# Optimization experiments

Measured on AMD Instinct MI355X. Metric: run time of the kernel, lower is better.

The kernel has to match this reference:

```python
import jax, jax.numpy as jnp
import numpy as np

HEADS = 8
DIM_HEAD = 32
SCALE = DIM_HEAD ** -0.5
EPS = 1e-5


def setup_inputs() -> dict:
    key = jax.random.key(0)
    k1, k2, k3 = jax.random.split(key, 3)
    b, dim, n = 8, 512, 8192
    hidden = HEADS * DIM_HEAD  # 256
    return {
        "x": jax.random.normal(k1, (b, dim, n), dtype=jnp.float32),
        "g": jnp.ones((1, dim, 1), dtype=jnp.float32),
        "b_ln": jnp.zeros((1, dim, 1), dtype=jnp.float32),
        "w_qkv": jax.random.normal(k2, (hidden * 3, dim), dtype=jnp.float32) * (dim ** -0.5),
        "w_out": jax.random.normal(k3, (dim, hidden), dtype=jnp.float32) * (hidden ** -0.5),
        "b_out": jnp.zeros((dim,), dtype=jnp.float32),
    }


def reference(x, g, b_ln, w_qkv, w_out, b_out):
    b, c, n = x.shape
    # channel LayerNorm (biased variance over dim=1)
    mean = jnp.mean(x, axis=1, keepdims=True)
    var = jnp.var(x, axis=1, keepdims=True)
    x_norm = (x - mean) / jnp.sqrt(var + EPS) * g + b_ln
    # 1x1 conv QKV projection: [3*hidden, c] x [b, c, n] -> [b, 3*hidden, n]
    qkv = jnp.einsum('oc,bcn->bon', w_qkv, x_norm)
    hidden = w_qkv.shape[0] // 3
    q, k, v = jnp.split(qkv, 3, axis=1)
    # [b, h, dh, n]
    q = q.reshape(b, HEADS, DIM_HEAD, n) * SCALE
    k = k.reshape(b, HEADS, DIM_HEAD, n)
    v = v.reshape(b, HEADS, DIM_HEAD, n)
    k = jax.nn.softmax(k, axis=-1)  # softmax over sequence positions
    # linear attention: context = k v^T  (dh x dh per head), then context q
    context = jnp.einsum('bhdn,bhen->bhde', k, v)
    out = jnp.einsum('bhde,bhdn->bhen', context, q)
    out = out.reshape(b, hidden, n)
    out = jnp.einsum('oc,bcn->bon', w_out, out) + b_out[None, :, None]
    return out + x
```

## Files before the change

kernel.cpp:

```cpp
#include <hip/hip_runtime.h>
#include <hip/hip_bf16.h>
#include <math.h>

#define HEADS 8
#define DH 32
#define BATCH 8
#define CDIM 512
#define NSEQ 8192
#define HID 256
#define O3 768
#define LNEPS 1e-5f
#define QSCALE 0.1767766952966369f

typedef __bf16 bf16x8 __attribute__((ext_vector_type(8)));
typedef float f32x4 __attribute__((ext_vector_type(4)));
typedef unsigned short u16;
typedef u16 u16x4 __attribute__((ext_vector_type(4)));
typedef u16 u16x8 __attribute__((ext_vector_type(8)));

__device__ __forceinline__ void gld_lds16(const void* g, void* l) {
  __builtin_amdgcn_global_load_lds(
      (const __attribute__((address_space(1))) unsigned int*)g,
      (__attribute__((address_space(3))) unsigned int*)l, 16, 0, 0);
}

__device__ __forceinline__ float ldx(const void* p, size_t i, bool f32) {
  if (f32) {
    float v = ((const float*)p)[i];
    return __builtin_isfinite(v) ? v : 0.f;
  }
  return __bfloat162float(((const __hip_bfloat16*)p)[i]);
}

__device__ __forceinline__ u16 b16(float v) {
  union { __hip_bfloat16 h; u16 u; } cv;
  cv.h = __float2bfloat16(v);
  return cv.u;
}

__device__ __forceinline__ float fb16(u16 u) {
  return __uint_as_float((unsigned)u << 16);
}

__device__ __forceinline__ void stage8(__hip_bfloat16* dst, const void* src, size_t idx, bool f32) {
  if (f32) {
    const float* s = (const float*)src + idx;
#pragma unroll
    for (int t = 0; t < 8; ++t) {
      float v = s[t];
      if (!__builtin_isfinite(v)) v = 0.f;
      dst[t] = __float2bfloat16(v);
    }
  } else {
    *(int4*)dst = *(const int4*)((const __hip_bfloat16*)src + idx);
  }
}

__device__ __forceinline__ void stx(void* p, size_t i, bool f32, float v) {
  if (!__builtin_isfinite(v)) v = 0.f;
  if (f32) ((float*)p)[i] = v;
  else ((__hip_bfloat16*)p)[i] = __float2bfloat16(v);
}

__global__ __launch_bounds__(256) void detect_kernel(const void* __restrict__ x, int* __restrict__ mode) {
  __shared__ int cnt;
  if (threadIdx.x == 0) cnt = 0;
  __syncthreads();
  const __hip_bfloat16* p = (const __hip_bfloat16*)x;
  int c = 0;
  for (int i = threadIdx.x; i < 4096; i += 256) {
    float v = __bfloat162float(p[i]);
    if (!(v > -1.0e3f && v < 1.0e3f)) c++;
  }
  atomicAdd(&cnt, c);
  __syncthreads();
  if (threadIdx.x == 0) mode[0] = (cnt > 64) ? 1 : 0;
}

__global__ __launch_bounds__(256) void ln_stats4_kernel(
    const void* __restrict__ x, const int* __restrict__ mode,
    float* __restrict__ mean, float* __restrict__ rstd) {
  const bool f32 = mode[0] != 0;
  const int b = blockIdx.y;
  const int n0 = blockIdx.x * 128;
  const int t = threadIdx.x;
  const int m = t & 31, cp = t >> 5;
  const int n4 = m * 4;
  const size_t base = (size_t)b * CDIM * NSEQ + n0 + n4;
  f32x4 s = {0.f, 0.f, 0.f, 0.f}, q = {0.f, 0.f, 0.f, 0.f};
  for (int c = cp * 64; c < cp * 64 + 64; ++c) {
    f32x4 v;
    if (f32) {
      v = *(const f32x4*)((const float*)x + base + (size_t)c * NSEQ);
#pragma unroll
      for (int j = 0; j < 4; ++j) if (!__builtin_isfinite(v[j])) v[j] = 0.f;
    } else {
      u16x4 h = *(const u16x4*)((const __hip_bfloat16*)x + base + (size_t)c * NSEQ);
#pragma unroll
      for (int j = 0; j < 4; ++j) v[j] = fb16(h[j]);
    }
    s += v;
    q += v * v;
  }
  __shared__ f32x4 sbS[8][32], sbQ[8][32];
  sbS[cp][m] = s; sbQ[cp][m] = q;
  __syncthreads();
  if (t < 32) {
    f32x4 S = sbS[0][t], Q = sbQ[0][t];
#pragma unroll
    for (int k = 1; k < 8; ++k) { S += sbS[k][t]; Q += sbQ[k][t]; }
    f32x4 M = S * (1.f / CDIM);
    f32x4 V = Q * (1.f / CDIM) - M * M;
#pragma unroll
    for (int j = 0; j < 4; ++j) {
      mean[b * NSEQ + n0 + t * 4 + j] = M[j];
      rstd[b * NSEQ + n0 + t * 4 + j] = rsqrtf(fmaxf(V[j], 0.f) + LNEPS);
    }
  }
}

__global__ __launch_bounds__(256) void wconv_kernel(
    const void* __restrict__ wqkv, const int* __restrict__ mode,
    __hip_bfloat16* __restrict__ wb) {
  const bool f32 = mode[0] != 0;
  const size_t i = ((size_t)blockIdx.x * 256 + threadIdx.x) * 8;
  if (f32) {
    f32x4 a = *(const f32x4*)((const float*)wqkv + i);
    f32x4 c = *(const f32x4*)((const float*)wqkv + i + 4);
    u16x8 o;
#pragma unroll
    for (int j = 0; j < 4; ++j) {
      float va = __builtin_isfinite(a[j]) ? a[j] : 0.f;
      float vc = __builtin_isfinite(c[j]) ? c[j] : 0.f;
      o[j] = b16(va);
      o[4 + j] = b16(vc);
    }
    *(u16x8*)&wb[i] = o;
  } else {
    *(int4*)&wb[i] = *(const int4*)((const __hip_bfloat16*)wqkv + i);
  }
}

__global__ __launch_bounds__(256) void xnormt_kernel(
    const void* __restrict__ x, const void* __restrict__ g, const void* __restrict__ bln,
    const int* __restrict__ mode, const float* __restrict__ mean, const float* __restrict__ rstd,
    __hip_bfloat16* __restrict__ xnt) {
  const bool f32 = mode[0] != 0;
  const int b = blockIdx.z;
  const int c0 = blockIdx.y * 128;
  const int n0 = blockIdx.x * 128;
  __shared__ u16 tile[128 * 132];
  const int t = threadIdx.x;
  const int m = t & 31, rb = t >> 5;
  const int n4 = m * 4;
  const f32x4 mn = *(const f32x4*)&mean[b * NSEQ + n0 + n4];
  const f32x4 rs = *(const f32x4*)&rstd[b * NSEQ + n0 + n4];
#pragma unroll
  for (int it = 0; it < 16; ++it) {
    const int r = it * 8 + rb;
    const float gv = ldx(g, c0 + r, f32);
    const float bv = ldx(bln, c0 + r, f32);
    const size_t src = ((size_t)b * CDIM + c0 + r) * NSEQ + n0 + n4;
    f32x4 v;
    if (f32) {
      v = *(const f32x4*)((const float*)x + src);
#pragma unroll
      for (int j = 0; j < 4; ++j) if (!__builtin_isfinite(v[j])) v[j] = 0.f;
    } else {
      u16x4 h = *(const u16x4*)((const __hip_bfloat16*)x + src);
#pragma unroll
      for (int j = 0; j < 4; ++j) v[j] = fb16(h[j]);
    }
    u16x4 o;
#pragma unroll
    for (int j = 0; j < 4; ++j) o[j] = b16((v[j] - mn[j]) * rs[j] * gv + bv);
    *(u16x4*)&tile[r * 132 + n4] = o;
  }
  __syncthreads();
  const int n = t >> 1, ch = t & 1;
  __hip_bfloat16* dst = xnt + ((size_t)b * NSEQ + n0 + n) * CDIM + c0 + ch * 64;
#pragma unroll
  for (int i8 = 0; i8 < 8; ++i8) {
    u16x8 o;
#pragma unroll
    for (int k = 0; k < 8; ++k) o[k] = tile[(ch * 64 + i8 * 8 + k) * 132 + n];
    *(u16x8*)(dst + i8 * 8) = o;
  }
}

__global__ __launch_bounds__(256) void ln_stats_kernel(
    const void* __restrict__ x, const int* __restrict__ mode,
    float* __restrict__ mean, float* __restrict__ rstd) {
  const bool f32 = mode[0] != 0;
  int b = blockIdx.y;
  int nl = threadIdx.x & 63;
  int cp = threadIdx.x >> 6;
  int n = blockIdx.x * 64 + nl;
  size_t base = (size_t)b * CDIM * NSEQ + n;
  float s = 0.f, ss = 0.f;
  for (int c = cp * 128; c < cp * 128 + 128; ++c) {
    float v = ldx(x, base + (size_t)c * NSEQ, f32);
    s += v; ss += v * v;
  }
  __shared__ float sb[4][64], sb2[4][64];
  sb[cp][nl] = s; sb2[cp][nl] = ss;
  __syncthreads();
  if (cp == 0) {
    s = sb[0][nl] + sb[1][nl] + sb[2][nl] + sb[3][nl];
    ss = sb2[0][nl] + sb2[1][nl] + sb2[2][nl] + sb2[3][nl];
    float m = s * (1.f / CDIM);
    float var = ss * (1.f / CDIM) - m * m;
    mean[b * NSEQ + n] = m;
    rstd[b * NSEQ + n] = rsqrtf(fmaxf(var, 0.f) + LNEPS);
  }
}

__global__ __launch_bounds__(512) void kv_gemm6_kernel(
    const __hip_bfloat16* __restrict__ wb, const __hip_bfloat16* __restrict__ xnt,
    float* __restrict__ ctxb, float* __restrict__ sumexp) {
  const int b = blockIdx.z;
  const int p = blockIdx.y;
  const int n0 = blockIdx.x * 256;
  __shared__ __align__(16) char smem[73728];
  __hip_bfloat16* Ct = (__hip_bfloat16*)smem;
  const int tid = threadIdx.x;
  const int lane = tid & 63;
  const int wv = tid >> 6;
  const int wm = wv >> 2, wn = wv & 3;
  const int quad = lane >> 4, l = lane & 15;
  f32x4 acc[4][4] = {};
  const __hip_bfloat16* xb = xnt + (size_t)b * NSEQ * CDIM;
  const int r16 = lane >> 2;
  const int cs8 = ((lane & 3) ^ (r16 & 3)) * 8;
  const int cq = (quad ^ (l & 3)) * 8;
  const int rowA = wv * 16 + r16;
  const int srowA = (rowA < 64) ? (256 + p * 64 + rowA) : (512 + p * 64 + (rowA - 64));
  const int rowB = wv * 32 + r16;

#define KV_STAGE(bufidx, k0) do {                                              \
    __hip_bfloat16* As_ = (__hip_bfloat16*)(smem + (bufidx) * 24576);          \
    __hip_bfloat16* Bs_ = As_ + 128 * 32;                                      \
    gld_lds16(&wb[(size_t)srowA * CDIM + (k0) + cs8], &As_[(wv * 16) * 32]);   \
    gld_lds16(&xb[(size_t)(n0 + rowB) * CDIM + (k0) + cs8],                    \
              &Bs_[(wv * 32) * 32]);                                           \
    gld_lds16(&xb[(size_t)(n0 + rowB + 16) * CDIM + (k0) + cs8],               \
              &Bs_[(wv * 32 + 16) * 32]);                                      \
  } while (0)

  KV_STAGE(0, 0);
  KV_STAGE(1, 32);
  for (int t = 0; t < 16; ++t) {
    if (t < 15) asm volatile("s_waitcnt vmcnt(3)" ::: "memory");
    else        asm volatile("s_waitcnt vmcnt(0)" ::: "memory");
    __builtin_amdgcn_s_barrier();
    __builtin_amdgcn_sched_barrier(0);
    if (t + 2 < 16) KV_STAGE((t + 2) % 3, (t + 2) * 32);
    const __hip_bfloat16* As = (const __hip_bfloat16*)(smem + (t % 3) * 24576);
    const __hip_bfloat16* Bs = As + 128 * 32;
    bf16x8 af[4], bfr[4];
#pragma unroll
    for (int i = 0; i < 4; ++i)
      af[i] = *(const bf16x8*)&As[(wm * 64 + i * 16 + l) * 32 + cq];
#pragma unroll
    for (int j = 0; j < 4; ++j)
      bfr[j] = *(const bf16x8*)&Bs[(wn * 64 + j * 16 + l) * 32 + cq];
#pragma unroll
    for (int i = 0; i < 4; ++i)
#pragma unroll
      for (int j = 0; j < 4; ++j)
        acc[i][j] = __builtin_amdgcn_mfma_f32_16x16x32_bf16(af[i], bfr[j], acc[i][j], 0, 0, 0);
  }
#undef KV_STAGE
  __syncthreads();
#pragma unroll
  for (int i = 0; i < 4; ++i) {
    int row = wm * 64 + i * 16 + quad * 4;
#pragma unroll
    for (int j = 0; j < 4; ++j) {
      int col = wn * 64 + j * 16 + l;
#pragma unroll
      for (int r = 0; r < 4; ++r) {
        float v = acc[i][j][r];
        if (wm == 0) v = expf(fminf(v, 20.f));
        else         v = fminf(fmaxf(v, -1.0e4f), 1.0e4f);
        Ct[(row + r) * 264 + col] = __float2bfloat16(v);
      }
    }
  }
  __syncthreads();
  const int mi = wm, ni = wn & 1, kh = wn >> 1;
#pragma unroll
  for (int hh = 0; hh < 2; ++hh) {
    f32x4 ca = {};
#pragma unroll
    for (int ks = 0; ks < 4; ++ks) {
      int kk = kh * 4 + ks;
      bf16x8 ea = *(const bf16x8*)&Ct[(hh * 32 + mi * 16 + l) * 264 + kk * 32 + quad * 8];
      bf16x8 vb = *(const bf16x8*)&Ct[(64 + hh * 32 + ni * 16 + l) * 264 + kk * 32 + quad * 8];
      ca = __builtin_amdgcn_mfma_f32_16x16x32_bf16(ea, vb, ca, 0, 0, 0);
    }
    int h = p * 2 + hh;
    float* cp = ctxb + (size_t)(b * HEADS + h) * DH * DH;
#pragma unroll
    for (int r = 0; r < 4; ++r)
      atomicAdd(&cp[(mi * 16 + quad * 4 + r) * DH + ni * 16 + l], ca[r]);
  }
  if (tid < 64) {
    int hh = tid >> 5, d = tid & 31;
    float s = 0.f;
#pragma unroll
    for (int c8 = 0; c8 < 32; ++c8) {
      u16x8 h8 = *(const u16x8*)&Ct[tid * 264 + c8 * 8];
#pragma unroll
      for (int k = 0; k < 8; ++k) s += fb16(h8[k]);
    }
    atomicAdd(&sumexp[(b * HEADS + p * 2 + hh) * DH + d], s);
  }
}

__global__ __launch_bounds__(256) void kvctx_kernel(
    const void* __restrict__ x, const void* __restrict__ g,
    const void* __restrict__ bln, const void* __restrict__ wqkv,
    const int* __restrict__ mode,
    const float* __restrict__ mean, const float* __restrict__ rstd,
    float* __restrict__ ctxb, float* __restrict__ sumexp) {
  const bool f32 = mode[0] != 0;
  const int b = blockIdx.z;
  const int p = blockIdx.y;
  const int n0 = blockIdx.x * 128;
  __shared__ __align__(16) __hip_bfloat16 As[128 * 32];
  __shared__ __align__(16) __hip_bfloat16 Bs[128 * 40];
  __shared__ __align__(16) __hip_bfloat16 Ct[128 * 136];
  const int tid = threadIdx.x;
  const int lane = tid & 63;
  const int wv = tid >> 6;
  const int wm = wv >> 1, wn = wv & 1;
  const int quad = lane >> 4, l = lane & 15;
  f32x4 acc[4][4] = {};
  const int nn = tid & 127;
  const int cb = tid >> 7;
  const float mn = mean[b * NSEQ + n0 + nn];
  const float rs = rstd[b * NSEQ + n0 + nn];
  const size_t xbase = (size_t)b * CDIM * NSEQ + n0 + nn;
  for (int k0 = 0; k0 < CDIM; k0 += 32) {
#pragma unroll
    for (int r = 0; r < 2; ++r) {
      int idx = (r * 256 + tid) * 8;
      int row = idx >> 5, col = idx & 31;
      int srow = (row < 64) ? (256 + p * 64 + row) : (512 + p * 64 + row - 64);
      stage8(&As[idx], wqkv, (size_t)srow * CDIM + k0 + col, f32);
    }
#pragma unroll
    for (int r = 0; r < 16; ++r) {
      int c = r * 2 + cb;
      float xv = ldx(x, xbase + (size_t)(k0 + c) * NSEQ, f32);
      float xn = (xv - mn) * rs;
      xn = xn * ldx(g, k0 + c, f32) + ldx(bln, k0 + c, f32);
      Bs[nn * 40 + c] = __float2bfloat16(xn);
    }
    __syncthreads();
    bf16x8 af[4], bfr[4];
#pragma unroll
    for (int i = 0; i < 4; ++i)
      af[i] = *(const bf16x8*)&As[(wm * 64 + i * 16 + l) * 32 + quad * 8];
#pragma unroll
    for (int j = 0; j < 4; ++j)
      bfr[j] = *(const bf16x8*)&Bs[(wn * 64 + j * 16 + l) * 40 + quad * 8];
#pragma unroll
    for (int i = 0; i < 4; ++i)
#pragma unroll
      for (int j = 0; j < 4; ++j)
        acc[i][j] = __builtin_amdgcn_mfma_f32_16x16x32_bf16(af[i], bfr[j], acc[i][j], 0, 0, 0);
    __syncthreads();
  }
#pragma unroll
  for (int i = 0; i < 4; ++i) {
    int row = wm * 64 + i * 16 + quad * 4;
#pragma unroll
    for (int j = 0; j < 4; ++j) {
      int col = wn * 64 + j * 16 + l;
#pragma unroll
      for (int r = 0; r < 4; ++r) {
        float v = acc[i][j][r];
        if (wm == 0) v = expf(fminf(v, 20.f));
        else         v = fminf(fmaxf(v, -1.0e4f), 1.0e4f);
        Ct[(row + r) * 136 + col] = __float2bfloat16(v);
      }
    }
  }
  __syncthreads();
  const int mi = wm, ni = wn;
#pragma unroll
  for (int hh = 0; hh < 2; ++hh) {
    f32x4 ca = {};
#pragma unroll
    for (int ks = 0; ks < 4; ++ks) {
      bf16x8 ea = *(const bf16x8*)&Ct[(hh * 32 + mi * 16 + l) * 136 + ks * 32 + quad * 8];
      bf16x8 vb = *(const bf16x8*)&Ct[(64 + hh * 32 + ni * 16 + l) * 136 + ks * 32 + quad * 8];
      ca = __builtin_amdgcn_mfma_f32_16x16x32_bf16(ea, vb, ca, 0, 0, 0);
    }
    int h = p * 2 + hh;
    float* cp = ctxb + (size_t)(b * HEADS + h) * DH * DH;
#pragma unroll
    for (int r = 0; r < 4; ++r)
      atomicAdd(&cp[(mi * 16 + quad * 4 + r) * DH + ni * 16 + l], ca[r]);
  }
  if (tid < 64) {
    int hh = tid >> 5, d = tid & 31;
    float s = 0.f;
#pragma unroll 16
    for (int c = 0; c < 128; ++c) s += __bfloat162float(Ct[tid * 136 + c]);
    atomicAdd(&sumexp[(b * HEADS + p * 2 + hh) * DH + d], s);
  }
}

__global__ __launch_bounds__(256) void w2_build_kernel(
    const void* __restrict__ wout, const int* __restrict__ mode,
    const float* __restrict__ ctxb, const float* __restrict__ sumexp,
    __hip_bfloat16* __restrict__ w2) {
  const bool f32 = mode[0] != 0;
  const int o = blockIdx.x;
  const int b = blockIdx.y;
  const int hd = threadIdx.x;
  const int h = hd >> 5, d = hd & 31;
  const float* cp = ctxb + ((size_t)(b * HEADS + h) * DH + d) * DH;
  float a = 0.f;
#pragma unroll
  for (int e = 0; e < DH; ++e) a += ldx(wout, (size_t)o * HID + h * DH + e, f32) * cp[e];
  float se = fmaxf(sumexp[(b * HEADS + h) * DH + d], 1e-30f);
  float v = a * QSCALE / se;
  v = fminf(fmaxf(v, -1.0e3f), 1.0e3f);
  w2[((size_t)b * CDIM + o) * HID + hd] = __float2bfloat16(v);
}

__global__ __launch_bounds__(256) void w3_gemm2_kernel(
    const __hip_bfloat16* __restrict__ w2, const __hip_bfloat16* __restrict__ wb,
    __hip_bfloat16* __restrict__ w3) {
  const int b = blockIdx.z;
  const int m0 = blockIdx.y * 128;
  const int n0 = blockIdx.x * 128;
  __shared__ __align__(16) __hip_bfloat16 As[128 * 40];
  __shared__ __align__(16) __hip_bfloat16 Bs[128 * 40];
  const int tid = threadIdx.x;
  const int lane = tid & 63;
  const int wv = tid >> 6;
  const int wm = wv >> 1, wn = wv & 1;
  const int quad = lane >> 4, l = lane & 15;
  f32x4 acc[4][4] = {};
  const int nn = tid & 127;
  const int cb = tid >> 7;
  const __hip_bfloat16* wa = w2 + (size_t)b * CDIM * HID;
  for (int k0 = 0; k0 < HID; k0 += 32) {
#pragma unroll
    for (int i = 0; i < 2; ++i) {
      int gid = tid + i * 256;
      int row = gid >> 2, c8 = (gid & 3) * 8;
      *(int4*)&As[row * 40 + c8] = *(const int4*)&wa[(size_t)(m0 + row) * HID + k0 + c8];
    }
#pragma unroll
    for (int r = 0; r < 16; ++r) {
      int hdl = r * 2 + cb;
      Bs[nn * 40 + hdl] = wb[(size_t)(k0 + hdl) * CDIM + n0 + nn];
    }
    __syncthreads();
    bf16x8 af[4], bfr[4];
#pragma unroll
    for (int i = 0; i < 4; ++i)
      af[i] = *(const bf16x8*)&As[(wm * 64 + i * 16 + l) * 40 + quad * 8];
#pragma unroll
    for (int j = 0; j < 4; ++j)
      bfr[j] = *(const bf16x8*)&Bs[(wn * 64 + j * 16 + l) * 40 + quad * 8];
#pragma unroll
    for (int i = 0; i < 4; ++i)
#pragma unroll
      for (int j = 0; j < 4; ++j)
        acc[i][j] = __builtin_amdgcn_mfma_f32_16x16x32_bf16(af[i], bfr[j], acc[i][j], 0, 0, 0);
    __syncthreads();
  }
#pragma unroll
  for (int i = 0; i < 4; ++i) {
    int orow = m0 + wm * 64 + i * 16 + quad * 4;
#pragma unroll
    for (int j = 0; j < 4; ++j) {
      int ncol = n0 + wn * 64 + j * 16 + l;
      __hip_bfloat16* op = w3 + ((size_t)b * CDIM + orow) * CDIM + ncol;
#pragma unroll
      for (int r = 0; r < 4; ++r) {
        float v = fminf(fmaxf(acc[i][j][r], -1.0e4f), 1.0e4f);
        op[(size_t)r * CDIM] = __float2bfloat16(v);
      }
    }
  }
}

__global__ __launch_bounds__(256) void w3_gemm_kernel(
    const __hip_bfloat16* __restrict__ w2, const void* __restrict__ wqkv,
    const int* __restrict__ mode, __hip_bfloat16* __restrict__ w3) {
  const bool f32 = mode[0] != 0;
  const int b = blockIdx.z;
  const int m0 = blockIdx.y * 128;
  const int n0 = blockIdx.x * 128;
  __shared__ __align__(16) __hip_bfloat16 As[128 * 32];
  __shared__ __align__(16) __hip_bfloat16 Bs[128 * 40];
  const int tid = threadIdx.x;
  const int lane = tid & 63;
  const int wv = tid >> 6;
  const int wm = wv >> 1, wn = wv & 1;
  const int quad = lane >> 4, l = lane & 15;
  f32x4 acc[4][4] = {};
  const int nn = tid & 127;
  const int cb = tid >> 7;
  const __hip_bfloat16* wa = w2 + (size_t)b * CDIM * HID;
  for (int k0 = 0; k0 < HID; k0 += 32) {
#pragma unroll
    for (int r = 0; r < 2; ++r) {
      int idx = (r * 256 + tid) * 8;
      int row = idx >> 5, col = idx & 31;
      *(int4*)&As[idx] = *(const int4*)&wa[(size_t)(m0 + row) * HID + k0 + col];
    }
#pragma unroll
    for (int r = 0; r < 16; ++r) {
      int hdl = r * 2 + cb;
      Bs[nn * 40 + hdl] = __float2bfloat16(ldx(wqkv, (size_t)(k0 + hdl) * CDIM + n0 + nn, f32));
    }
    __syncthreads();
    bf16x8 af[4], bfr[4];
#pragma unroll
    for (int i = 0; i < 4; ++i)
      af[i] = *(const bf16x8*)&As[(wm * 64 + i * 16 + l) * 32 + quad * 8];
#pragma unroll
    for (int j = 0; j < 4; ++j)
      bfr[j] = *(const bf16x8*)&Bs[(wn * 64 + j * 16 + l) * 40 + quad * 8];
#pragma unroll
    for (int i = 0; i < 4; ++i)
#pragma unroll
      for (int j = 0; j < 4; ++j)
        acc[i][j] = __builtin_amdgcn_mfma_f32_16x16x32_bf16(af[i], bfr[j], acc[i][j], 0, 0, 0);
    __syncthreads();
  }
#pragma unroll
  for (int i = 0; i < 4; ++i) {
    int orow = m0 + wm * 64 + i * 16 + quad * 4;
#pragma unroll
    for (int j = 0; j < 4; ++j) {
      int ncol = n0 + wn * 64 + j * 16 + l;
      __hip_bfloat16* op = w3 + ((size_t)b * CDIM + orow) * CDIM + ncol;
#pragma unroll
      for (int r = 0; r < 4; ++r) {
        float v = fminf(fmaxf(acc[i][j][r], -1.0e4f), 1.0e4f);
        op[(size_t)r * CDIM] = __float2bfloat16(v);
      }
    }
  }
}

__global__ __launch_bounds__(512) void out_gemm6_kernel(
    const void* __restrict__ x, const __hip_bfloat16* __restrict__ w3,
    const __hip_bfloat16* __restrict__ xnt, const int* __restrict__ mode,
    const void* __restrict__ bout, void* __restrict__ out) {
  const bool f32 = mode[0] != 0;
  const int b = blockIdx.z;
  const int m0 = blockIdx.y * 128;
  const int n0 = blockIdx.x * 256;
  __shared__ __align__(16) char smem[73728];
  const int tid = threadIdx.x;
  const int lane = tid & 63;
  const int wv = tid >> 6;
  const int wm = wv >> 2, wn = wv & 3;
  const int quad = lane >> 4, l = lane & 15;
  f32x4 acc[4][4] = {};
  const __hip_bfloat16* wa = w3 + (size_t)b * CDIM * CDIM;
  const __hip_bfloat16* xb = xnt + (size_t)b * NSEQ * CDIM;
  const int r16 = lane >> 2;
  const int cs8 = ((lane & 3) ^ (r16 & 3)) * 8;
  const int cq = (quad ^ (l & 3)) * 8;
  const int rowA = wv * 16 + r16;
  const int rowB = wv * 32 + r16;

#define OUT_STAGE(bufidx, k0) do {                                             \
    __hip_bfloat16* As_ = (__hip_bfloat16*)(smem + (bufidx) * 24576);          \
    __hip_bfloat16* Bs_ = As_ + 128 * 32;                                      \
    gld_lds16(&wa[(size_t)(m0 + rowA) * CDIM + (k0) + cs8],                    \
              &As_[(wv * 16) * 32]);                                           \
    gld_lds16(&xb[(size_t)(n0 + rowB) * CDIM + (k0) + cs8],                    \
              &Bs_[(wv * 32) * 32]);                                           \
    gld_lds16(&xb[(size_t)(n0 + rowB + 16) * CDIM + (k0) + cs8],               \
              &Bs_[(wv * 32 + 16) * 32]);                                      \
  } while (0)

  OUT_STAGE(0, 0);
  OUT_STAGE(1, 32);
  for (int t = 0; t < 16; ++t) {
    if (t < 15) asm volatile("s_waitcnt vmcnt(3)" ::: "memory");
    else        asm volatile("s_waitcnt vmcnt(0)" ::: "memory");
    __builtin_amdgcn_s_barrier();
    __builtin_amdgcn_sched_barrier(0);
    if (t + 2 < 16) OUT_STAGE((t + 2) % 3, (t + 2) * 32);
    const __hip_bfloat16* As = (const __hip_bfloat16*)(smem + (t % 3) * 24576);
    const __hip_bfloat16* Bs = As + 128 * 32;
    bf16x8 af[4], bfr[4];
#pragma unroll
    for (int i = 0; i < 4; ++i)
      af[i] = *(const bf16x8*)&As[(wm * 64 + i * 16 + l) * 32 + cq];
#pragma unroll
    for (int j = 0; j < 4; ++j)
      bfr[j] = *(const bf16x8*)&Bs[(wn * 64 + j * 16 + l) * 32 + cq];
#pragma unroll
    for (int i = 0; i < 4; ++i)
#pragma unroll
      for (int j = 0; j < 4; ++j)
        acc[i][j] = __builtin_amdgcn_mfma_f32_16x16x32_bf16(af[i], bfr[j], acc[i][j], 0, 0, 0);
  }
#undef OUT_STAGE
#pragma unroll
  for (int i = 0; i < 4; ++i) {
    int orow = m0 + wm * 64 + i * 16 + quad * 4;
#pragma unroll
    for (int j = 0; j < 4; ++j) {
      int ncol = n0 + wn * 64 + j * 16 + l;
#pragma unroll
      for (int r = 0; r < 4; ++r) {
        size_t oi = ((size_t)b * CDIM + orow + r) * NSEQ + ncol;
        float v = acc[i][j][r] + ldx(bout, orow + r, f32) + ldx(x, oi, f32);
        stx(out, oi, f32, v);
      }
    }
  }
}

__global__ __launch_bounds__(256) void out_gemm_kernel(
    const void* __restrict__ x, const void* __restrict__ g,
    const void* __restrict__ bln, const __hip_bfloat16* __restrict__ w3,
    const int* __restrict__ mode,
    const float* __restrict__ mean, const float* __restrict__ rstd,
    const void* __restrict__ bout, void* __restrict__ out) {
  const bool f32 = mode[0] != 0;
  const int b = blockIdx.z;
  const int m0 = blockIdx.y * 128;
  const int n0 = blockIdx.x * 128;
  __shared__ __align__(16) __hip_bfloat16 As[128 * 32];
  __shared__ __align__(16) __hip_bfloat16 Bs[128 * 40];
  const int tid = threadIdx.x;
  const int lane = tid & 63;
  const int wv = tid >> 6;
  const int wm = wv >> 1, wn = wv & 1;
  const int quad = lane >> 4, l = lane & 15;
  f32x4 acc[4][4] = {};
  const int nn = tid & 127;
  const int cb = tid >> 7;
  const float mn = mean[b * NSEQ + n0 + nn];
  const float rs = rstd[b * NSEQ + n0 + nn];
  const size_t xbase = (size_t)b * CDIM * NSEQ + n0 + nn;
  const __hip_bfloat16* wa = w3 + (size_t)b * CDIM * CDIM;
  for (int k0 = 0; k0 < CDIM; k0 += 32) {
#pragma unroll
    for (int r = 0; r < 2; ++r) {
      int idx = (r * 256 + tid) * 8;
      int row = idx >> 5, col = idx & 31;
      *(int4*)&As[idx] = *(const int4*)&wa[(size_t)(m0 + row) * CDIM + k0 + col];
    }
#pragma unroll
    for (int r = 0; r < 16; ++r) {
      int c = r * 2 + cb;
      float xv = ldx(x, xbase + (size_t)(k0 + c) * NSEQ, f32);
      float xn = (xv - mn) * rs;
      xn = xn * ldx(g, k0 + c, f32) + ldx(bln, k0 + c, f32);
      Bs[nn * 40 + c] = __float2bfloat16(xn);
    }
    __syncthreads();
    bf16x8 af[4], bfr[4];
#pragma unroll
    for (int i = 0; i < 4; ++i)
      af[i] = *(const bf16x8*)&As[(wm * 64 + i * 16 + l) * 32 + quad * 8];
#pragma unroll
    for (int j = 0; j < 4; ++j)
      bfr[j] = *(const bf16x8*)&Bs[(wn * 64 + j * 16 + l) * 40 + quad * 8];
#pragma unroll
    for (int i = 0; i < 4; ++i)
#pragma unroll
      for (int j = 0; j < 4; ++j)
        acc[i][j] = __builtin_amdgcn_mfma_f32_16x16x32_bf16(af[i], bfr[j], acc[i][j], 0, 0, 0);
    __syncthreads();
  }
#pragma unroll
  for (int i = 0; i < 4; ++i) {
    int orow = m0 + wm * 64 + i * 16 + quad * 4;
#pragma unroll
    for (int j = 0; j < 4; ++j) {
      int ncol = n0 + wn * 64 + j * 16 + l;
#pragma unroll
      for (int r = 0; r < 4; ++r) {
        size_t oi = ((size_t)b * CDIM + orow + r) * NSEQ + ncol;
        float v = acc[i][j][r] + ldx(bout, orow + r, f32) + ldx(x, oi, f32);
        stx(out, oi, f32, v);
      }
    }
  }
}

extern "C" void kernel_launch(void* const* d_in, const int* in_sizes, int n_in,
                              void* d_out, int out_size, void* d_ws, size_t ws_size,
                              hipStream_t stream) {
  (void)in_sizes; (void)n_in; (void)out_size;
  const void* x    = d_in[0];
  const void* g    = d_in[1];
  const void* bln  = d_in[2];
  const void* wqkv = d_in[3];
  const void* wout = d_in[4];
  const void* bout = d_in[5];

  float* mean   = (float*)d_ws;
  float* rstd   = mean + BATCH * NSEQ;
  float* ctxb   = rstd + BATCH * NSEQ;
  float* sumexp = ctxb + BATCH * HEADS * DH * DH;
  int*   mode   = (int*)(sumexp + BATCH * HEADS * DH);
  __hip_bfloat16* w2  = (__hip_bfloat16*)(mode + 64);
  __hip_bfloat16* w3  = w2 + (size_t)BATCH * CDIM * HID;
  __hip_bfloat16* wb  = w3 + (size_t)BATCH * CDIM * CDIM;
  __hip_bfloat16* xnt = wb + (size_t)O3 * CDIM;
  const size_t need = (size_t)((const char*)(xnt + (size_t)BATCH * NSEQ * CDIM) - (const char*)d_ws);

  hipMemsetAsync(ctxb, 0, (BATCH * HEADS * DH * DH + BATCH * HEADS * DH) * sizeof(float), stream);
  detect_kernel<<<1, 256, 0, stream>>>(x, mode);

  if (ws_size >= need) {
    ln_stats4_kernel<<<dim3(NSEQ / 128, BATCH), 256, 0, stream>>>(x, mode, mean, rstd);
    wconv_kernel<<<dim3((O3 * CDIM) / 2048), 256, 0, stream>>>(wqkv, mode, wb);
    xnormt_kernel<<<dim3(NSEQ / 128, CDIM / 128, BATCH), 256, 0, stream>>>(
        x, g, bln, mode, mean, rstd, xnt);
    kv_gemm6_kernel<<<dim3(NSEQ / 256, HEADS / 2, BATCH), 512, 0, stream>>>(
        wb, xnt, ctxb, sumexp);
    w2_build_kernel<<<dim3(CDIM, BATCH), 256, 0, stream>>>(wout, mode, ctxb, sumexp, w2);
    w3_gemm2_kernel<<<dim3(CDIM / 128, CDIM / 128, BATCH), 256, 0, stream>>>(w2, wb, w3);
    out_gemm6_kernel<<<dim3(NSEQ / 256, CDIM / 128, BATCH), 512, 0, stream>>>(
        x, w3, xnt, mode, bout, d_out);
  } else {
    ln_stats_kernel<<<dim3(NSEQ / 64, BATCH), 256, 0, stream>>>(x, mode, mean, rstd);
    kvctx_kernel<<<dim3(NSEQ / 128, HEADS / 2, BATCH), 256, 0, stream>>>(
        x, g, bln, wqkv, mode, mean, rstd, ctxb, sumexp);
    w2_build_kernel<<<dim3(CDIM, BATCH), 256, 0, stream>>>(wout, mode, ctxb, sumexp, w2);
    w3_gemm_kernel<<<dim3(CDIM / 128, CDIM / 128, BATCH), 256, 0, stream>>>(w2, wqkv, mode, w3);
    out_gemm_kernel<<<dim3(NSEQ / 128, CDIM / 128, BATCH), 256, 0, stream>>>(
        x, g, bln, w3, mode, mean, rstd, bout, d_out);
  }
}
```

Measured before the change: 547.4 us.

## Keep full A panel resident in LDS and stream B fragments from global

The output GEMM now loads the whole 64x512 slice of the per-batch W3 matrix into LDS once, using an XOR swizzle, with a single barrier. Each wave then reads its B (normalized x) fragments straight from global memory into registers instead of going through a triple-buffered LDS pipeline. Tiles change to 64 rows by 512 columns, and each wave owns 64 columns. This removes the per-step barriers and staging of B, at the cost of unhidden global latency on the B loads and less reuse of B across waves, since each wave's B data is read by only that wave.

```diff
diff --git a/kernel.cpp b/kernel.cpp
--- a/kernel.cpp
+++ b/kernel.cpp
@@ -554,74 +554,59 @@
   }
 }
 
-__global__ __launch_bounds__(512) void out_gemm6_kernel(
+__global__ __launch_bounds__(512) void out_gemm7_kernel(
     const void* __restrict__ x, const __hip_bfloat16* __restrict__ w3,
     const __hip_bfloat16* __restrict__ xnt, const int* __restrict__ mode,
     const void* __restrict__ bout, void* __restrict__ out) {
   const bool f32 = mode[0] != 0;
   const int b = blockIdx.z;
-  const int m0 = blockIdx.y * 128;
-  const int n0 = blockIdx.x * 256;
-  __shared__ __align__(16) char smem[73728];
+  const int m0 = blockIdx.y * 64;
+  const int n0 = blockIdx.x * 512;
+  __shared__ __align__(16) __hip_bfloat16 As[64 * 512];
   const int tid = threadIdx.x;
   const int lane = tid & 63;
   const int wv = tid >> 6;
-  const int wm = wv >> 2, wn = wv & 3;
   const int quad = lane >> 4, l = lane & 15;
-  f32x4 acc[4][4] = {};
   const __hip_bfloat16* wa = w3 + (size_t)b * CDIM * CDIM;
   const __hip_bfloat16* xb = xnt + (size_t)b * NSEQ * CDIM;
-  const int r16 = lane >> 2;
-  const int cs8 = ((lane & 3) ^ (r16 & 3)) * 8;
-  const int cq = (quad ^ (l & 3)) * 8;
-  const int rowA = wv * 16 + r16;
-  const int rowB = wv * 32 + r16;
-
-#define OUT_STAGE(bufidx, k0) do {                                             \
-    __hip_bfloat16* As_ = (__hip_bfloat16*)(smem + (bufidx) * 24576);          \
-    __hip_bfloat16* Bs_ = As_ + 128 * 32;                                      \
-    gld_lds16(&wa[(size_t)(m0 + rowA) * CDIM + (k0) + cs8],                    \
-              &As_[(wv * 16) * 32]);                                           \
-    gld_lds16(&xb[(size_t)(n0 + rowB) * CDIM + (k0) + cs8],                    \
-              &Bs_[(wv * 32) * 32]);                                           \
-    gld_lds16(&xb[(size_t)(n0 + rowB + 16) * CDIM + (k0) + cs8],               \
-              &Bs_[(wv * 32 + 16) * 32]);                                      \
-  } while (0)
-
-  OUT_STAGE(0, 0);
-  OUT_STAGE(1, 32);
+#pragma unroll
+  for (int j = 0; j < 8; ++j) {
+    int row = wv * 8 + j;
+    int schunk = lane ^ (row & 7);
+    gld_lds16(&wa[(size_t)(m0 + row) * CDIM + schunk * 8], &As[row * 512]);
+  }
+  __syncthreads();
+  f32x4 acc[4][4] = {};
+  const int nw = n0 + wv * 64;
+#pragma unroll 2
   for (int t = 0; t < 16; ++t) {
-    if (t < 15) asm volatile("s_waitcnt vmcnt(3)" ::: "memory");
-    else        asm volatile("s_waitcnt vmcnt(0)" ::: "memory");
-    __builtin_amdgcn_s_barrier();
-    __builtin_amdgcn_sched_barrier(0);
-    if (t + 2 < 16) OUT_STAGE((t + 2) % 3, (t + 2) * 32);
-    const __hip_bfloat16* As = (const __hip_bfloat16*)(smem + (t % 3) * 24576);
-    const __hip_bfloat16* Bs = As + 128 * 32;
-    bf16x8 af[4], bfr[4];
-#pragma unroll
-    for (int i = 0; i < 4; ++i)
-      af[i] = *(const bf16x8*)&As[(wm * 64 + i * 16 + l) * 32 + cq];
-#pragma unroll
-    for (int j = 0; j < 4; ++j)
-      bfr[j] = *(const bf16x8*)&Bs[(wn * 64 + j * 16 + l) * 32 + cq];
-#pragma unroll
-    for (int i = 0; i < 4; ++i)
-#pragma unroll
-      for (int j = 0; j < 4; ++j)
-        acc[i][j] = __builtin_amdgcn_mfma_f32_16x16x32_bf16(af[i], bfr[j], acc[i][j], 0, 0, 0);
-  }
-#undef OUT_STAGE
+    const int k0 = t * 32;
+    bf16x8 bfr[4], af[4];
+#pragma unroll
+    for (int nf = 0; nf < 4; ++nf)
+      bfr[nf] = *(const bf16x8*)&xb[(size_t)(nw + nf * 16 + l) * CDIM + k0 + quad * 8];
+#pragma unroll
+    for (int i = 0; i < 4; ++i) {
+      int row = i * 16 + l;
+      int chunk = (t * 4 + quad) ^ (row & 7);
+      af[i] = *(const bf16x8*)&As[row * 512 + chunk * 8];
+    }
+#pragma unroll
+    for (int i = 0; i < 4; ++i)
+#pragma unroll
+      for (int nf = 0; nf < 4; ++nf)
+        acc[i][nf] = __builtin_amdgcn_mfma_f32_16x16x32_bf16(af[i], bfr[nf], acc[i][nf], 0, 0, 0);
+  }
 #pragma unroll
   for (int i = 0; i < 4; ++i) {
-    int orow = m0 + wm * 64 + i * 16 + quad * 4;
-#pragma unroll
-    for (int j = 0; j < 4; ++j) {
-      int ncol = n0 + wn * 64 + j * 16 + l;
+    int orow = m0 + i * 16 + quad * 4;
+#pragma unroll
+    for (int nf = 0; nf < 4; ++nf) {
+      int ncol = nw + nf * 16 + l;
 #pragma unroll
       for (int r = 0; r < 4; ++r) {
         size_t oi = ((size_t)b * CDIM + orow + r) * NSEQ + ncol;
-        float v = acc[i][j][r] + ldx(bout, orow + r, f32) + ldx(x, oi, f32);
+        float v = acc[i][nf][r] + ldx(bout, orow + r, f32) + ldx(x, oi, f32);
         stx(out, oi, f32, v);
       }
     }
@@ -732,7 +717,7 @@
         wb, xnt, ctxb, sumexp);
     w2_build_kernel<<<dim3(CDIM, BATCH), 256, 0, stream>>>(wout, mode, ctxb, sumexp, w2);
     w3_gemm2_kernel<<<dim3(CDIM / 128, CDIM / 128, BATCH), 256, 0, stream>>>(w2, wb, w3);
-    out_gemm6_kernel<<<dim3(NSEQ / 256, CDIM / 128, BATCH), 512, 0, stream>>>(
+    out_gemm7_kernel<<<dim3(NSEQ / 512, CDIM / 64, BATCH), 512, 0, stream>>>(
         x, w3, xnt, mode, bout, d_out);
   } else {
     ln_stats_kernel<<<dim3(NSEQ / 64, BATCH), 256, 0, stream>>>(x, mode, mean, rstd);
```

Result: slower. 579.5 us (+5.9%).
